# Kernel tuning notes

Measured on AMD Instinct MI355X. Metric: run time of the kernel, lower is better.

Reference implementation:

```python
import jax, jax.numpy as jnp
import numpy as np

EPS = 1e-8  # torch cosine_similarity eps


def setup_inputs() -> dict:
    key = jax.random.key(0)
    kx, kw = jax.random.split(key)
    B, D, C, K = 512, 512, 5994, 3
    x = jax.random.normal(kx, (B, D), dtype=jnp.float32)
    # xavier_normal over (D, C, K): std = sqrt(2 / (fan_in + fan_out))
    std = float(np.sqrt(2.0 / (D + C * K)))
    W = jax.random.normal(kw, (D, C, K), dtype=jnp.float32) * std
    return {"x": x, "W": W}


def reference(x, W):
    # cosine similarity along feature dim, without materializing [B, D, C, K]
    x_norm = jnp.maximum(jnp.linalg.norm(x, axis=1, keepdims=True), EPS)   # [B, 1]
    w_norm = jnp.maximum(jnp.linalg.norm(W, axis=0, keepdims=True), EPS)   # [1, C, K]
    xn = x / x_norm                                                        # [B, D]
    Wn = W / w_norm                                                        # [D, C, K]
    costh = jnp.einsum('bd,dck->bck', xn, Wn)                              # [B, C, K]
    return costh
```

## Files before the change

kernel.cpp:

```cpp
#include <hip/hip_runtime.h>
#include <hip/hip_bf16.h>
#include <stdint.h>


#define D_DIM 512
#define BM 128
#define BN 128
#define KITERS 16
#define TILE_BYTES (64 * BM * 16)

typedef __bf16 bf16x8 __attribute__((ext_vector_type(8)));
typedef float f32x4 __attribute__((ext_vector_type(4)));

__device__ __forceinline__ unsigned short f2bf(float f) {
  union { float f; unsigned int u; } v; v.f = f;
  unsigned int u = v.u;
  u += 0x7fffu + ((u >> 16) & 1u);
  return (unsigned short)(u >> 16);
}

__device__ __forceinline__ void load_lds16(const void* g, void* l) {
  __builtin_amdgcn_global_load_lds(
      (__attribute__((address_space(1))) void*)(g),
      (__attribute__((address_space(3))) void*)(l), 16, 0, 0);
}

__global__ void prep_kernel(const float* __restrict__ x, const float* __restrict__ W,
                            unsigned short* __restrict__ An, unsigned short* __restrict__ Wt,
                            float* __restrict__ partial, int CK, int NT128, int nWtBlocks) {
  const int b = blockIdx.x;
  const int t = threadIdx.x;
  if (b < nWtBlocks) {
    __shared__ float red[8 * 128];
    const int ntile = b >> 3, gb = b & 7;
    const int cq = t & 31, dr = t >> 5;
    const int n0 = ntile * BN;
    const int nb = n0 + cq * 4;
    const int g = gb * 8 + dr;
    float ss0 = 0.f, ss1 = 0.f, ss2 = 0.f, ss3 = 0.f;
    unsigned int gr[4][4];
    if (n0 + BN <= CK) {
#pragma unroll
      for (int i = 0; i < 8; i += 2) {
        float4 v0 = *(const float4*)(W + (size_t)(g * 8 + i) * CK + nb);
        float4 v1 = *(const float4*)(W + (size_t)(g * 8 + i + 1) * CK + nb);
        ss0 += v0.x * v0.x + v1.x * v1.x; ss1 += v0.y * v0.y + v1.y * v1.y;
        ss2 += v0.z * v0.z + v1.z * v1.z; ss3 += v0.w * v0.w + v1.w * v1.w;
        gr[0][i >> 1] = (unsigned int)f2bf(v0.x) | ((unsigned int)f2bf(v1.x) << 16);
        gr[1][i >> 1] = (unsigned int)f2bf(v0.y) | ((unsigned int)f2bf(v1.y) << 16);
        gr[2][i >> 1] = (unsigned int)f2bf(v0.z) | ((unsigned int)f2bf(v1.z) << 16);
        gr[3][i >> 1] = (unsigned int)f2bf(v0.w) | ((unsigned int)f2bf(v1.w) << 16);
      }
    } else {
      float acc_ss[4] = {0.f, 0.f, 0.f, 0.f};
#pragma unroll
      for (int i = 0; i < 8; i += 2) {
#pragma unroll
        for (int e = 0; e < 4; ++e) {
          const int n = nb + e;
          const float f0 = (n < CK) ? W[(size_t)(g * 8 + i) * CK + n] : 0.f;
          const float f1 = (n < CK) ? W[(size_t)(g * 8 + i + 1) * CK + n] : 0.f;
          acc_ss[e] += f0 * f0 + f1 * f1;
          gr[e][i >> 1] = (unsigned int)f2bf(f0) | ((unsigned int)f2bf(f1) << 16);
        }
      }
      ss0 = acc_ss[0]; ss1 = acc_ss[1]; ss2 = acc_ss[2]; ss3 = acc_ss[3];
    }
    unsigned short* dst = Wt + (size_t)ntile * (TILE_BYTES / 2) + (size_t)g * (BM * 8) + (size_t)cq * 32;
#pragma unroll
    for (int e = 0; e < 4; ++e) {
      uint4 o; o.x = gr[e][0]; o.y = gr[e][1]; o.z = gr[e][2]; o.w = gr[e][3];
      *(uint4*)(dst + e * 8) = o;
    }
    *(float4*)(&red[dr * 128 + cq * 4]) = make_float4(ss0, ss1, ss2, ss3);
    __syncthreads();
    if (t < 128) {
      float s = 0.f;
#pragma unroll
      for (int k = 0; k < 8; ++k) s += red[k * 128 + t];
      partial[(size_t)gb * NT128 + n0 + t] = s;
    }
  } else {
    const int w = t >> 6, lane = t & 63;
    const int m = (b - nWtBlocks) * 4 + w;
    const float* xr = x + (size_t)m * D_DIM + lane * 8;
    float4 a = *(const float4*)(xr);
    float4 c = *(const float4*)(xr + 4);
    float s = a.x * a.x + a.y * a.y + a.z * a.z + a.w * a.w +
              c.x * c.x + c.y * c.y + c.z * c.z + c.w * c.w;
#pragma unroll
    for (int off = 32; off; off >>= 1) s += __shfl_xor(s, off, 64);
    const float inv = 1.f / fmaxf(sqrtf(s), 1e-8f);
    ushort4 o0, o1;
    o0.x = f2bf(a.x * inv); o0.y = f2bf(a.y * inv); o0.z = f2bf(a.z * inv); o0.w = f2bf(a.w * inv);
    o1.x = f2bf(c.x * inv); o1.y = f2bf(c.y * inv); o1.z = f2bf(c.z * inv); o1.w = f2bf(c.w * inv);
    const int mtile = m >> 7, r = m & 127;
    unsigned short* dst = An + (size_t)mtile * (TILE_BYTES / 2) + (size_t)lane * (BM * 8) + r * 8;
    *(ushort4*)dst = o0;
    *(ushort4*)(dst + 4) = o1;
  }
}

__global__ __launch_bounds__(256, 3) void gemm_kernel(const unsigned short* __restrict__ An,
                                                      const unsigned short* __restrict__ Wt,
                                                      const float* __restrict__ partial,
                                                      float* __restrict__ out, int CK, int NT128) {
  __shared__ __attribute__((aligned(16))) unsigned char lds[49152];
  const int total = gridDim.x;
  const int q = total >> 3, rr = total & 7;
  const int lin = blockIdx.x;
  const int xcd = lin & 7, idx = lin >> 3;
  const int wg = ((xcd < rr) ? xcd * (q + 1) : rr * (q + 1) + (xcd - rr) * q) + idx;
  const int ntile = wg >> 2, mtile = wg & 3;

  const int t = threadIdx.x;
  const int lane = t & 63, w = t >> 6;
  const int wm = w >> 1, wn = w & 1;
  const int lrow = lane & 15;
  const int kg = lane >> 4;

  const unsigned char* srcA = (const unsigned char*)An + (size_t)mtile * TILE_BYTES;
  const unsigned char* srcB = (const unsigned char*)Wt + (size_t)ntile * TILE_BYTES;
  const int n0 = ntile * BN;
  const bool full = (n0 + BN <= CK);

  f32x4 acc[4][4] = {};

#define STAGE(kt, sel)                                                        \
  {                                                                           \
    const size_t koff = (size_t)(kt) * 8192;                                  \
    unsigned char* bAw = lds + (sel) * 16384;                                 \
    unsigned char* bBw = bAw + 8192;                                          \
    _Pragma("unroll")                                                         \
    for (int c = 0; c < 2; ++c) {                                             \
      const int off = c * 4096 + t * 16;                                      \
      load_lds16(srcA + koff + off, bAw + off);                               \
    }                                                                         \
    _Pragma("unroll")                                                         \
    for (int c = 0; c < 2; ++c) {                                             \
      const int off = c * 4096 + t * 16;                                      \
      load_lds16(srcB + koff + off, bBw + off);                               \
    }                                                                         \
  }

  STAGE(0, 0);

#pragma unroll
  for (int kt = 0; kt < KITERS; ++kt) {
    if (kt + 1 < KITERS) STAGE(kt + 1, (kt + 1) % 3);
    __builtin_amdgcn_sched_barrier(0);
    if (kt + 1 < KITERS) {
      asm volatile("s_waitcnt vmcnt(4)" ::: "memory");
    } else {
      asm volatile("s_waitcnt vmcnt(0)" ::: "memory");
    }
    __builtin_amdgcn_s_barrier();
    __builtin_amdgcn_sched_barrier(0);

    const unsigned char* bA = lds + (kt % 3) * 16384;
    const unsigned char* bB = bA + 8192;
    bf16x8 afrag[4], bfrag[4];
#pragma unroll
    for (int i = 0; i < 4; ++i) {
      afrag[i] = *(const bf16x8*)(bA + kg * 2048 + (wm * 64 + i * 16 + lrow) * 16);
      bfrag[i] = *(const bf16x8*)(bB + kg * 2048 + (wn * 64 + i * 16 + lrow) * 16);
    }
#pragma unroll
    for (int i = 0; i < 4; ++i)
#pragma unroll
      for (int j = 0; j < 4; ++j)
        acc[i][j] = __builtin_amdgcn_mfma_f32_16x16x32_bf16(afrag[i], bfrag[j], acc[i][j], 0, 0, 0);
  }

  __syncthreads();
  float* winv = (float*)lds;
  if (t < 128) {
    float s = 0.f;
#pragma unroll
    for (int k = 0; k < 8; ++k) s += partial[(size_t)k * NT128 + n0 + t];
    winv[t] = 1.f / fmaxf(sqrtf(s), 1e-8f);
  }
  __syncthreads();
  float wv[4];
#pragma unroll
  for (int j = 0; j < 4; ++j) wv[j] = winv[wn * 64 + j * 16 + lrow];

  if (full) {
    float* stg = (float*)(lds + 1024) + w * 2176;
    const int l15 = lane & 15, l4 = lane >> 4;
#pragma unroll
    for (int half = 0; half < 2; ++half) {
#pragma unroll
      for (int di = 0; di < 2; ++di)
#pragma unroll
        for (int j = 0; j < 4; ++j)
#pragma unroll
          for (int jj = 0; jj < 4; ++jj)
            stg[(di * 16 + kg * 4 + jj) * 68 + j * 16 + lrow] = acc[half * 2 + di][j][jj] * wv[j];
#pragma unroll
      for (int s = 0; s < 8; ++s) {
        const int rl = s * 4 + l4;
        float4 v = *(float4*)&stg[rl * 68 + l15 * 4];
        const int row = mtile * BM + wm * 64 + half * 32 + rl;
        *(float4*)&out[(size_t)row * CK + n0 + wn * 64 + l15 * 4] = v;
      }
    }
  } else {
#pragma unroll
    for (int j = 0; j < 4; ++j) {
      const int col = n0 + wn * 64 + j * 16 + lrow;
      if (col < CK) {
#pragma unroll
        for (int i = 0; i < 4; ++i)
#pragma unroll
          for (int jj = 0; jj < 4; ++jj) {
            const int row = mtile * BM + wm * 64 + i * 16 + kg * 4 + jj;
            out[(size_t)row * CK + col] = acc[i][j][jj] * wv[j];
          }
      }
    }
  }
}

extern "C" void kernel_launch(void* const* d_in, const int* in_sizes, int n_in,
                              void* d_out, int out_size, void* d_ws, size_t ws_size,
                              hipStream_t stream) {
  const float* x = (const float*)d_in[0];
  const float* W = (const float*)d_in[1];
  float* out = (float*)d_out;
  const int Bn = in_sizes[0] / D_DIM;
  const int CK = in_sizes[1] / D_DIM;
  const int ntiles = (CK + BN - 1) / BN;
  const int mtiles = Bn / BM;
  const int NT128 = ntiles * BN;

  unsigned char* ws = (unsigned char*)d_ws;
  float* partial = (float*)ws;
  unsigned short* An = (unsigned short*)(ws + 8 * (size_t)NT128 * 4);
  unsigned short* Wt = (unsigned short*)(ws + 8 * (size_t)NT128 * 4 + (size_t)mtiles * TILE_BYTES);

  const int nWtBlocks = ntiles * 8;
  const int nXBlocks = Bn / 4;
  hipLaunchKernelGGL(prep_kernel, dim3(nWtBlocks + nXBlocks), dim3(256), 0, stream,
                     x, W, An, Wt, partial, CK, NT128, nWtBlocks);
  hipLaunchKernelGGL(gemm_kernel, dim3(ntiles * mtiles), dim3(256), 0, stream,
                     An, Wt, partial, out, CK, NT128);
}
```

Measured before the change: 35.88 us.

## Deepen GEMM LDS pipeline to four buffers, prefetch two ahead, raise MFMA priority

```diff
diff --git a/kernel.cpp b/kernel.cpp
--- a/kernel.cpp
+++ b/kernel.cpp
@@ -10,13 +10,12 @@
 #define TILE_BYTES (64 * BM * 16)
 
 typedef __bf16 bf16x8 __attribute__((ext_vector_type(8)));
+typedef __bf16 bf16x2 __attribute__((ext_vector_type(2)));
 typedef float f32x4 __attribute__((ext_vector_type(4)));
 
-__device__ __forceinline__ unsigned short f2bf(float f) {
-  union { float f; unsigned int u; } v; v.f = f;
-  unsigned int u = v.u;
-  u += 0x7fffu + ((u >> 16) & 1u);
-  return (unsigned short)(u >> 16);
+__device__ __forceinline__ unsigned pk(float a, float b) {
+  bf16x2 t; t[0] = (__bf16)a; t[1] = (__bf16)b;
+  return __builtin_bit_cast(unsigned, t);
 }
 
 __device__ __forceinline__ void load_lds16(const void* g, void* l) {
@@ -46,10 +45,10 @@
         float4 v1 = *(const float4*)(W + (size_t)(g * 8 + i + 1) * CK + nb);
         ss0 += v0.x * v0.x + v1.x * v1.x; ss1 += v0.y * v0.y + v1.y * v1.y;
         ss2 += v0.z * v0.z + v1.z * v1.z; ss3 += v0.w * v0.w + v1.w * v1.w;
-        gr[0][i >> 1] = (unsigned int)f2bf(v0.x) | ((unsigned int)f2bf(v1.x) << 16);
-        gr[1][i >> 1] = (unsigned int)f2bf(v0.y) | ((unsigned int)f2bf(v1.y) << 16);
-        gr[2][i >> 1] = (unsigned int)f2bf(v0.z) | ((unsigned int)f2bf(v1.z) << 16);
-        gr[3][i >> 1] = (unsigned int)f2bf(v0.w) | ((unsigned int)f2bf(v1.w) << 16);
+        gr[0][i >> 1] = pk(v0.x, v1.x);
+        gr[1][i >> 1] = pk(v0.y, v1.y);
+        gr[2][i >> 1] = pk(v0.z, v1.z);
+        gr[3][i >> 1] = pk(v0.w, v1.w);
       }
     } else {
       float acc_ss[4] = {0.f, 0.f, 0.f, 0.f};
@@ -61,7 +60,7 @@
           const float f0 = (n < CK) ? W[(size_t)(g * 8 + i) * CK + n] : 0.f;
           const float f1 = (n < CK) ? W[(size_t)(g * 8 + i + 1) * CK + n] : 0.f;
           acc_ss[e] += f0 * f0 + f1 * f1;
-          gr[e][i >> 1] = (unsigned int)f2bf(f0) | ((unsigned int)f2bf(f1) << 16);
+          gr[e][i >> 1] = pk(f0, f1);
         }
       }
       ss0 = acc_ss[0]; ss1 = acc_ss[1]; ss2 = acc_ss[2]; ss3 = acc_ss[3];
@@ -92,8 +91,12 @@
     for (int off = 32; off; off >>= 1) s += __shfl_xor(s, off, 64);
     const float inv = 1.f / fmaxf(sqrtf(s), 1e-8f);
     ushort4 o0, o1;
-    o0.x = f2bf(a.x * inv); o0.y = f2bf(a.y * inv); o0.z = f2bf(a.z * inv); o0.w = f2bf(a.w * inv);
-    o1.x = f2bf(c.x * inv); o1.y = f2bf(c.y * inv); o1.z = f2bf(c.z * inv); o1.w = f2bf(c.w * inv);
+    const unsigned p0 = pk(a.x * inv, a.y * inv), p1 = pk(a.z * inv, a.w * inv);
+    const unsigned p2 = pk(c.x * inv, c.y * inv), p3 = pk(c.z * inv, c.w * inv);
+    o0.x = (unsigned short)(p0 & 0xffff); o0.y = (unsigned short)(p0 >> 16);
+    o0.z = (unsigned short)(p1 & 0xffff); o0.w = (unsigned short)(p1 >> 16);
+    o1.x = (unsigned short)(p2 & 0xffff); o1.y = (unsigned short)(p2 >> 16);
+    o1.z = (unsigned short)(p3 & 0xffff); o1.w = (unsigned short)(p3 >> 16);
     const int mtile = m >> 7, r = m & 127;
     unsigned short* dst = An + (size_t)mtile * (TILE_BYTES / 2) + (size_t)lane * (BM * 8) + r * 8;
     *(ushort4*)dst = o0;
@@ -101,11 +104,11 @@
   }
 }
 
-__global__ __launch_bounds__(256, 3) void gemm_kernel(const unsigned short* __restrict__ An,
+__global__ __launch_bounds__(256, 2) void gemm_kernel(const unsigned short* __restrict__ An,
                                                       const unsigned short* __restrict__ Wt,
                                                       const float* __restrict__ partial,
                                                       float* __restrict__ out, int CK, int NT128) {
-  __shared__ __attribute__((aligned(16))) unsigned char lds[49152];
+  __shared__ __attribute__((aligned(16))) unsigned char lds[65536];
   const int total = gridDim.x;
   const int q = total >> 3, rr = total & 7;
   const int lin = blockIdx.x;
@@ -144,12 +147,15 @@
   }
 
   STAGE(0, 0);
+  STAGE(1, 1);
 
 #pragma unroll
   for (int kt = 0; kt < KITERS; ++kt) {
-    if (kt + 1 < KITERS) STAGE(kt + 1, (kt + 1) % 3);
+    if (kt + 2 < KITERS) STAGE(kt + 2, (kt + 2) & 3);
     __builtin_amdgcn_sched_barrier(0);
-    if (kt + 1 < KITERS) {
+    if (kt + 2 < KITERS) {
+      asm volatile("s_waitcnt vmcnt(8)" ::: "memory");
+    } else if (kt + 1 < KITERS) {
       asm volatile("s_waitcnt vmcnt(4)" ::: "memory");
     } else {
       asm volatile("s_waitcnt vmcnt(0)" ::: "memory");
@@ -157,7 +163,7 @@
     __builtin_amdgcn_s_barrier();
     __builtin_amdgcn_sched_barrier(0);
 
-    const unsigned char* bA = lds + (kt % 3) * 16384;
+    const unsigned char* bA = lds + (kt & 3) * 16384;
     const unsigned char* bB = bA + 8192;
     bf16x8 afrag[4], bfrag[4];
 #pragma unroll
@@ -165,11 +171,13 @@
       afrag[i] = *(const bf16x8*)(bA + kg * 2048 + (wm * 64 + i * 16 + lrow) * 16);
       bfrag[i] = *(const bf16x8*)(bB + kg * 2048 + (wn * 64 + i * 16 + lrow) * 16);
     }
+    __builtin_amdgcn_s_setprio(1);
 #pragma unroll
     for (int i = 0; i < 4; ++i)
 #pragma unroll
       for (int j = 0; j < 4; ++j)
         acc[i][j] = __builtin_amdgcn_mfma_f32_16x16x32_bf16(afrag[i], bfrag[j], acc[i][j], 0, 0, 0);
+    __builtin_amdgcn_s_setprio(0);
   }
 
   __syncthreads();
@@ -220,6 +228,7 @@
       }
     }
   }
+#undef STAGE
 }
 
 extern "C" void kernel_launch(void* const* d_in, const int* in_sizes, int n_in,
```

After: 38.32 us. 6.8% more time.
